# Performance work log

Measured on AMD Instinct MI355X. Metric: run time of the kernel, lower is better.

Reference implementation:

```python
import jax, jax.numpy as jnp
import numpy as np

LAMBDA_A = 1.0
NUM_ITER = 3
K = 64
BN_EPS = 1e-5


def setup_inputs() -> dict:
    key = jax.random.key(0)
    ks = jax.random.split(key, 8)
    B, C, H, W = 16, 512, 64, 64
    x = jax.random.normal(ks[0], (B, C, H, W), dtype=jnp.float32)
    # codebook mu: init normal(std~sqrt(2/k)) then L2-normalize along dim=1 (k axis), as in torch init
    mu = jax.random.normal(ks[1], (C, K), dtype=jnp.float32) * np.sqrt(2.0 / K)
    mu = mu / jnp.maximum(jnp.linalg.norm(mu, axis=1, keepdims=True), 1e-12)
    # 1x1 convs expressed as (out, in) matrices
    stem_w = jax.random.normal(ks[2], (C, C), dtype=jnp.float32) * np.sqrt(2.0 / C)
    stem_b = jnp.zeros((C,), dtype=jnp.float32)
    head_w = jax.random.normal(ks[3], (C, C), dtype=jnp.float32) * np.sqrt(2.0 / C)
    head_b = jnp.zeros((C,), dtype=jnp.float32)
    bn_gamma = jnp.ones((C,), dtype=jnp.float32)
    bn_beta = jnp.zeros((C,), dtype=jnp.float32)
    return {"x": x, "mu": mu, "stem_w": stem_w, "stem_b": stem_b,
            "head_w": head_w, "head_b": head_b,
            "bn_gamma": bn_gamma, "bn_beta": bn_beta}


def _conv1x1(x, w, b):
    # x: (B,C,H,W), w: (O,C)
    return jnp.einsum('bchw,oc->bohw', x, w) + b[None, :, None, None]


def reference(x, mu, stem_w, stem_b, head_w, head_b, bn_gamma, bn_beta):
    B, C, H, W = x.shape
    N = H * W
    y = _conv1x1(x, stem_w, stem_b)                 # (B,C,H,W)
    yf = y.reshape(B, C, N).transpose(0, 2, 1)      # (B,N,C)

    mu_b = jnp.broadcast_to(mu[None], (B, C, K))    # (B,C,K)
    z = None
    for _ in range(NUM_ITER):
        z = jax.nn.softmax(LAMBDA_A * jnp.einsum('bnc,bck->bnk', yf, mu_b), axis=2)
        zn = z / (1e-6 + z.sum(axis=1, keepdims=True))
        mu_b = jnp.einsum('bnc,bnk->bck', yf, zn)
        mu_b = mu_b / jnp.maximum(jnp.linalg.norm(mu_b, axis=1, keepdims=True), 1e-12)

    # EM loop runs under no_grad in torch
    mu_b = jax.lax.stop_gradient(mu_b)
    z = jax.lax.stop_gradient(z)

    y2 = jnp.einsum('bck,bnk->bcn', mu_b, z).reshape(B, C, H, W)

    # head: ReLU -> 1x1 conv -> BatchNorm2d (training-mode batch stats)
    h = _conv1x1(jnp.maximum(y2, 0.0), head_w, head_b)
    mean = h.mean(axis=(0, 2, 3), keepdims=True)
    var = h.var(axis=(0, 2, 3), keepdims=True)
    h = (h - mean) * jax.lax.rsqrt(var + BN_EPS)
    h = h * bn_gamma[None, :, None, None] + bn_beta[None, :, None, None]

    return jnp.maximum(h + x, 0.0)
```

## Files before the change

### kernel.cpp

```cpp
#include <hip/hip_runtime.h>


typedef _Float16 half_t;
typedef _Float16 half4 __attribute__((ext_vector_type(4)));
typedef _Float16 half8 __attribute__((ext_vector_type(8)));
typedef float f32x4 __attribute__((ext_vector_type(4)));

#define GLD_LDS(gp, lp) __builtin_amdgcn_global_load_lds( \
    (const __attribute__((address_space(1))) void*)(gp),  \
    (__attribute__((address_space(3))) void*)(lp), 16, 0, 0)

#define SBAR __builtin_amdgcn_sched_barrier(0)
#define RAWBAR do { SBAR; __builtin_amdgcn_s_barrier(); SBAR; } while (0)
#define VM0   do { asm volatile("s_waitcnt vmcnt(0)" ::: "memory"); SBAR; } while (0)

constexpr int CB = 16;
constexpr int CC = 512;
constexpr int CN = 4096;
constexpr int CKK = 64;
constexpr long MALL = (long)CB * CN;

__device__ inline int swz8(int bid, int n) {
  return (bid & 7) * (n >> 3) + (bid >> 3);
}

__global__ __launch_bounds__(256) void prep(
    const float* __restrict__ stem_w, const float* __restrict__ head_w,
    const float* __restrict__ mu,
    half_t* __restrict__ swh, half_t* __restrict__ hwh,
    half_t* __restrict__ muT, half_t* __restrict__ muck)
{
  int i = blockIdx.x * 256 + threadIdx.x;
  swh[i] = (half_t)stem_w[i];
  hwh[i] = (half_t)head_w[i];
  if (i < CC * CKK) {
    int c = i >> 6, k = i & 63;
    half_t v = (half_t)mu[i];
    for (int b = 0; b < CB; ++b) {
      muT[(long)b * CKK * CC + (long)k * CC + c] = v;
      muck[(long)b * CC * CKK + i] = v;
    }
  }
}

__global__ __launch_bounds__(256) void xpose(
    const float* __restrict__ in, half_t* __restrict__ outT)
{
  __shared__ half_t t[64][65];
  const int s0 = blockIdx.x * 64, r0 = blockIdx.y * 64;
  const long bz = blockIdx.z;
  const float* ib = in + bz * (long)CC * CN;
  half_t* ob = outT + bz * (long)CC * CN;
  const int tid = threadIdx.x, cl = tid & 63, rw = tid >> 6;
#pragma unroll
  for (int it = 0; it < 16; ++it) {
    int r = it * 4 + rw;
    t[cl][r] = (half_t)ib[(long)(r0 + r) * CN + s0 + cl];
  }
  __syncthreads();
#pragma unroll
  for (int it = 0; it < 16; ++it) {
    int s = it * 4 + rw;
    ob[(long)(s0 + s) * CC + r0 + cl] = t[s][cl];
  }
}

template <int BM, int BN, int MODE, int EPI, bool SWZ, bool STATS>
__global__ __launch_bounds__(256) void gemm_abt(
    const half_t* __restrict__ A, const half_t* __restrict__ Bm,
    half_t* __restrict__ Co, half_t* __restrict__ CoT,
    float* __restrict__ Cacc, const float* __restrict__ bias,
    float* __restrict__ stats,
    int M, int Nn, int Kk, int ksplit, long sA, long sB, long sC)
{
  constexpr int FM = BM / 32, FN = BN / 32;
  constexpr int HB = (BM + BN) * 64;
  constexpr int EPS = (EPI != 0) ? BN * (BM + 4) : 0;
  constexpr int TOT = HB > EPS ? HB : EPS;
  __shared__ __align__(16) half_t smem[TOT];

  const int tid = threadIdx.x, wid = tid >> 6, lane = tid & 63;
  int bid = blockIdx.x;
  if constexpr (SWZ) bid = swz8(bid, gridDim.x);
  const int tilesN = Nn / BN;
  const int tm = bid / tilesN, tn = bid % tilesN;
  const long bz = blockIdx.z;
  const half_t* Ab = A + bz * sA + (long)tm * BM * Kk;
  const half_t* Bb = Bm + bz * sB + (long)tn * BN * Kk;
  const int ksteps = Kk >> 6;
  const int per = ksteps / ksplit;
  const int ks0 = blockIdx.y * per, ks1 = ks0 + per;
  const int wr = wid >> 1, wc = wid & 1;

  const int r8 = lane >> 3;
  const int gcs = ((lane & 7) ^ r8) * 8;

  auto stage = [&](int ks) {
    half_t* dA = smem;
    half_t* dB = smem + BM * 64;
    const half_t* ga = Ab + (long)ks * 64;
#pragma unroll
    for (int c = wid; c < BM / 8; c += 4)
      GLD_LDS(ga + (long)(c * 8 + r8) * Kk + gcs, &dA[c * 512]);
    const half_t* gb = Bb + (long)ks * 64;
#pragma unroll
    for (int c = wid; c < BN / 8; c += 4)
      GLD_LDS(gb + (long)(c * 8 + r8) * Kk + gcs, &dB[c * 512]);
  };

  f32x4 acc[FM][FN];
#pragma unroll
  for (int i = 0; i < FM; ++i)
#pragma unroll
    for (int j = 0; j < FN; ++j) acc[i][j] = f32x4{0.f, 0.f, 0.f, 0.f};

  for (int ks = ks0; ks < ks1; ++ks) {
    stage(ks);
    VM0;
    RAWBAR;
    const half_t* lA = smem;
    const half_t* lB = smem + BM * 64;
#pragma unroll
    for (int kk = 0; kk < 2; ++kk) {
      half8 af[FM], bfr[FN];
      const int cg = kk * 4 + (lane >> 4);
#pragma unroll
      for (int i = 0; i < FM; ++i) {
        const int rA = wr * (BM / 2) + i * 16 + (lane & 15);
        af[i] = *(const half8*)&lA[rA * 64 + ((cg ^ (rA & 7)) << 3)];
      }
#pragma unroll
      for (int j = 0; j < FN; ++j) {
        const int rB = wc * (BN / 2) + j * 16 + (lane & 15);
        bfr[j] = *(const half8*)&lB[rB * 64 + ((cg ^ (rB & 7)) << 3)];
      }
      __builtin_amdgcn_s_setprio(1);
#pragma unroll
      for (int i = 0; i < FM; ++i)
#pragma unroll
        for (int j = 0; j < FN; ++j)
          acc[i][j] = __builtin_amdgcn_mfma_f32_16x16x32_f16(af[i], bfr[j],
                                                             acc[i][j], 0, 0, 0);
      __builtin_amdgcn_s_setprio(0);
    }
    RAWBAR;
  }

  if constexpr (EPI != 0) {
    static_assert(BM == 128 && BN == 128, "LDS epilogue assumes 128x128");
    constexpr int PIT = BM + 4;
    half_t* ep = smem;
#pragma unroll
    for (int j = 0; j < FN; ++j) {
      const int nl = wc * 64 + j * 16 + (lane & 15);
      float bv = 0.f;
      if constexpr (MODE & 1) bv = bias[tn * BN + nl];
      float s1 = 0.f, s2 = 0.f;
#pragma unroll
      for (int i = 0; i < FM; ++i) {
        const int ml = wr * 64 + i * 16 + ((lane >> 4) << 2);
        half4 h;
#pragma unroll
        for (int r = 0; r < 4; ++r) {
          float v = acc[i][j][r] + bv;
          if constexpr (MODE & 2) v = fmaxf(v, 0.f);
          if constexpr (STATS) { s1 += v; s2 += v * v; }
          h[r] = (half_t)v;
        }
        *(half4*)&ep[nl * PIT + ml] = h;
      }
      if constexpr (STATS) {
        s1 += __shfl_xor(s1, 16); s1 += __shfl_xor(s1, 32);
        s2 += __shfl_xor(s2, 16); s2 += __shfl_xor(s2, 32);
        if (lane < 16) {
          const int ch = tn * BN + nl;
          atomicAdd(&stats[ch], s1);
          atomicAdd(&stats[CC + ch], s2);
        }
      }
    }
    __syncthreads();
    const long rowbase = (long)tm * BM;
    if constexpr (EPI & 1) {
#pragma unroll
      for (int s = 0; s < 8; ++s) {
        const int q = tid + 256 * s;
        const int m = q & 127, cc8 = q >> 7;
        half8 v;
#pragma unroll
        for (int e = 0; e < 8; ++e) v[e] = ep[(cc8 * 8 + e) * PIT + m];
        *(half8*)&Co[bz * sC + (rowbase + m) * Nn + tn * BN + cc8 * 8] = v;
      }
    }
    if constexpr (EPI & 2) {
      const long b = rowbase >> 12, nbase = rowbase & 4095;
#pragma unroll
      for (int s = 0; s < 8; ++s) {
        const int q = tid + 256 * s;
        const int mc = q & 15, cl = q >> 4;
        half8 v = *(const half8*)&ep[cl * PIT + mc * 8];
        *(half8*)&CoT[(b * Nn + tn * BN + cl) * 4096 + nbase + mc * 8] = v;
      }
    }
  } else {
#pragma unroll
    for (int j = 0; j < FN; ++j) {
      const int n = tn * BN + wc * (BN / 2) + j * 16 + (lane & 15);
      float bv = 0.f;
      if constexpr (MODE & 1) bv = bias[n];
#pragma unroll
      for (int i = 0; i < FM; ++i) {
        const int mbase = tm * BM + wr * (BM / 2) + i * 16 + ((lane >> 4) << 2);
#pragma unroll
        for (int r = 0; r < 4; ++r) {
          const long idx = bz * sC + (long)(mbase + r) * Nn + n;
          if constexpr ((MODE & 4) != 0) {
            atomicAdd(&Cacc[idx], acc[i][j][r]);
          } else {
            float v = acc[i][j][r] + bv;
            if constexpr ((MODE & 2) != 0) v = fmaxf(v, 0.f);
            Co[idx] = (half_t)v;
          }
        }
      }
    }
  }
}

__global__ __launch_bounds__(256) void s_softmax(
    const half_t* __restrict__ Yf, const half_t* __restrict__ muT,
    half_t* __restrict__ zp, half_t* __restrict__ zT)
{
  constexpr int HB = (128 + 64) * 64;
  __shared__ __align__(16) union {
    half_t st[HB];
    half_t zh[128 * 68];
  } sm;
  const int tid = threadIdx.x, wid = tid >> 6, lane = tid & 63;
  const int tm = blockIdx.x;
  const long bz = blockIdx.z;
  const half_t* Ab = Yf + bz * (long)CN * CC + (long)tm * 128 * CC;
  const half_t* Bb = muT + bz * (long)CKK * CC;

  const int r8 = lane >> 3;
  const int gcs = ((lane & 7) ^ r8) * 8;

  auto stage = [&](int ks) {
    half_t* dA = sm.st;
    half_t* dB = sm.st + 128 * 64;
    const half_t* ga = Ab + (long)ks * 64;
#pragma unroll
    for (int c = wid; c < 16; c += 4)
      GLD_LDS(ga + (long)(c * 8 + r8) * CC + gcs, &dA[c * 512]);
    const half_t* gb = Bb + (long)ks * 64;
#pragma unroll
    for (int c = wid; c < 8; c += 4)
      GLD_LDS(gb + (long)(c * 8 + r8) * CC + gcs, &dB[c * 512]);
  };

  f32x4 acc[2][4];
#pragma unroll
  for (int i = 0; i < 2; ++i)
#pragma unroll
    for (int j = 0; j < 4; ++j) acc[i][j] = f32x4{0.f, 0.f, 0.f, 0.f};

  for (int ks = 0; ks < 8; ++ks) {
    stage(ks);
    VM0;
    RAWBAR;
    const half_t* lA = sm.st;
    const half_t* lB = sm.st + 128 * 64;
#pragma unroll
    for (int kk = 0; kk < 2; ++kk) {
      half8 af[2], bfr[4];
      const int cg = kk * 4 + (lane >> 4);
#pragma unroll
      for (int i = 0; i < 2; ++i) {
        const int rA = wid * 32 + i * 16 + (lane & 15);
        af[i] = *(const half8*)&lA[rA * 64 + ((cg ^ (rA & 7)) << 3)];
      }
#pragma unroll
      for (int j = 0; j < 4; ++j) {
        const int rB = j * 16 + (lane & 15);
        bfr[j] = *(const half8*)&lB[rB * 64 + ((cg ^ (rB & 7)) << 3)];
      }
      __builtin_amdgcn_s_setprio(1);
#pragma unroll
      for (int i = 0; i < 2; ++i)
#pragma unroll
        for (int j = 0; j < 4; ++j)
          acc[i][j] = __builtin_amdgcn_mfma_f32_16x16x32_f16(af[i], bfr[j],
                                                             acc[i][j], 0, 0, 0);
      __builtin_amdgcn_s_setprio(0);
    }
    RAWBAR;
  }

#pragma unroll
  for (int i = 0; i < 2; ++i)
#pragma unroll
    for (int r = 0; r < 4; ++r) {
      float mx = fmaxf(fmaxf(acc[i][0][r], acc[i][1][r]),
                       fmaxf(acc[i][2][r], acc[i][3][r]));
#pragma unroll
      for (int m = 1; m < 16; m <<= 1) mx = fmaxf(mx, __shfl_xor(mx, m));
      float p[4], s = 0.f;
#pragma unroll
      for (int j = 0; j < 4; ++j) { p[j] = __expf(acc[i][j][r] - mx); s += p[j]; }
#pragma unroll
      for (int m = 1; m < 16; m <<= 1) s += __shfl_xor(s, m);
      const float inv = 1.f / s;
#pragma unroll
      for (int j = 0; j < 4; ++j) acc[i][j][r] = p[j] * inv;
    }

#pragma unroll
  for (int i = 0; i < 2; ++i)
#pragma unroll
    for (int j = 0; j < 4; ++j)
#pragma unroll
      for (int r = 0; r < 4; ++r) {
        const int row = wid * 32 + i * 16 + ((lane >> 4) << 2) + r;
        const int col = j * 16 + (lane & 15);
        sm.zh[row * 68 + col] = (half_t)acc[i][j][r];
      }
  __syncthreads();
  if (zp) {
    const int nl = tid >> 1, seg = tid & 1;
    const long base = bz * (long)CN * CKK + (long)(tm * 128 + nl) * CKK + seg * 32;
#pragma unroll
    for (int g = 0; g < 4; ++g) {
      half8 v;
#pragma unroll
      for (int e = 0; e < 8; ++e) v[e] = sm.zh[nl * 68 + seg * 32 + g * 8 + e];
      *(half8*)&zp[base + g * 8] = v;
    }
  }
  {
    const int k = tid >> 2, seg = tid & 3;
    const long base = bz * (long)CKK * CN + (long)k * CN + tm * 128 + seg * 32;
#pragma unroll
    for (int g = 0; g < 4; ++g) {
      half8 v;
#pragma unroll
      for (int e = 0; e < 8; ++e) v[e] = sm.zh[(seg * 32 + g * 8 + e) * 68 + k];
      *(half8*)&zT[base + g * 8] = v;
    }
  }
}

__global__ __launch_bounds__(64) void mu_norm(
    const float* __restrict__ acc, half_t* __restrict__ muT, half_t* __restrict__ muck)
{
  const int bk = blockIdx.x;
  const int b = bk >> 6, k = bk & 63;
  const float* row = acc + (long)bk * CC;
  const int t = threadIdx.x;
  float v[8]; float s = 0.f;
#pragma unroll
  for (int e = 0; e < 8; ++e) { v[e] = row[t * 8 + e]; s += v[e] * v[e]; }
#pragma unroll
  for (int m = 1; m < 64; m <<= 1) s += __shfl_xor(s, m);
  const float inv = 1.f / fmaxf(sqrtf(s), 1e-12f);
  half8 o;
#pragma unroll
  for (int e = 0; e < 8; ++e) o[e] = (half_t)(v[e] * inv);
  *(half8*)&muT[(long)bk * CC + t * 8] = o;
  half_t* mc = muck + (long)b * CC * CKK;
#pragma unroll
  for (int e = 0; e < 8; ++e) mc[(long)(t * 8 + e) * CKK + k] = o[e];
}

__global__ void bn_param(const float* __restrict__ stats,
                         const float* __restrict__ gamma, const float* __restrict__ beta,
                         float* __restrict__ scsh)
{
  const int c = threadIdx.x;
  const float cnt = 1.f / 65536.f;
  const float mean = stats[c] * cnt;
  const float var = stats[CC + c] * cnt - mean * mean;
  const float sc = gamma[c] * rsqrtf(var + 1e-5f);
  scsh[c] = sc;
  scsh[CC + c] = beta[c] - mean * sc;
}

__global__ __launch_bounds__(256) void bn_final2(
    const half_t* __restrict__ hcn, const float* __restrict__ x,
    const float* __restrict__ scsh, float* __restrict__ out)
{
  const long i8 = (long)blockIdx.x * 256 + threadIdx.x;
  const int c = (int)((i8 >> 9) & 511);
  const float sc = scsh[c], sh = scsh[CC + c];
  half8 h = *(const half8*)&hcn[i8 * 8];
  f32x4 x0 = *(const f32x4*)&x[i8 * 8];
  f32x4 x1 = *(const f32x4*)&x[i8 * 8 + 4];
  f32x4 o0, o1;
#pragma unroll
  for (int e = 0; e < 4; ++e) o0[e] = fmaxf((float)h[e] * sc + sh + x0[e], 0.f);
#pragma unroll
  for (int e = 0; e < 4; ++e) o1[e] = fmaxf((float)h[4 + e] * sc + sh + x1[e], 0.f);
  *(f32x4*)&out[i8 * 8] = o0;
  *(f32x4*)&out[i8 * 8 + 4] = o1;
}

extern "C" void kernel_launch(void* const* d_in, const int* in_sizes, int n_in,
                              void* d_out, int out_size, void* d_ws, size_t ws_size,
                              hipStream_t stream)
{
  const float* x      = (const float*)d_in[0];
  const float* mu     = (const float*)d_in[1];
  const float* stem_w = (const float*)d_in[2];
  const float* stem_b = (const float*)d_in[3];
  const float* head_w = (const float*)d_in[4];
  const float* head_b = (const float*)d_in[5];
  const float* bn_g   = (const float*)d_in[6];
  const float* bn_b   = (const float*)d_in[7];
  float* out = (float*)d_out;

  const size_t NEED = 214ull << 20;
  if (ws_size < NEED) {
    hipMemsetAsync(d_out, 0, (size_t)out_size * 4, stream);
    return;
  }
  char* ws = (char*)d_ws;
  const long MB = 1 << 20;
  half_t* xT   = (half_t*)(ws);
  half_t* Yf   = (half_t*)(ws + 64 * MB);
  half_t* ycn  = (half_t*)(ws + 128 * MB);
  half_t* z    = (half_t*)(ws + 192 * MB);
  half_t* zT   = (half_t*)(ws + 200 * MB);
  half_t* muT  = (half_t*)(ws + 208 * MB);
  half_t* muck = (half_t*)(ws + 209 * MB);
  float* muacc = (float*)(ws + 210 * MB);
  half_t* swh  = (half_t*)(ws + 212 * MB);
  half_t* hwh  = (half_t*)(ws + 212 * MB + 512 * 1024);
  float* stats = (float*)(ws + 213 * MB);
  float* scsh  = (float*)(ws + 213 * MB + 8 * 1024);
  half_t* y2f = xT;
  half_t* hcn = Yf;

  prep<<<1024, 256, 0, stream>>>(stem_w, head_w, mu, swh, hwh, muT, muck);
  xpose<<<dim3(64, 8, 16), 256, 0, stream>>>(x, xT);
  gemm_abt<128, 128, 1, 3, true, false><<<dim3(2048, 1, 1), 256, 0, stream>>>(
      xT, swh, Yf, ycn, nullptr, stem_b, nullptr, (int)MALL, CC, CC, 1, 0, 0, 0);

  for (int it = 0; it < 3; ++it) {
    s_softmax<<<dim3(32, 1, 16), 256, 0, stream>>>(
        Yf, muT, (it == 2) ? z : nullptr, zT);
    hipMemsetAsync(muacc, 0, (size_t)CB * CKK * CC * 4, stream);
    gemm_abt<64, 128, 4, 0, false, false><<<dim3(4, 8, 16), 256, 0, stream>>>(
        zT, ycn, nullptr, nullptr, muacc, nullptr, nullptr, CKK, CC, CN, 8,
        (long)CKK * CN, (long)CC * CN, (long)CKK * CC);
    mu_norm<<<CB * CKK, 64, 0, stream>>>(muacc, muT, muck);
  }
  gemm_abt<128, 128, 2, 1, true, false><<<dim3(128, 1, 16), 256, 0, stream>>>(
      z, muck, y2f, nullptr, nullptr, nullptr, nullptr, CN, CC, CKK, 1,
      (long)CN * CKK, (long)CC * CKK, (long)CN * CC);
  hipMemsetAsync(stats, 0, 2 * CC * sizeof(float), stream);
  gemm_abt<128, 128, 1, 2, true, true><<<dim3(2048, 1, 1), 256, 0, stream>>>(
      y2f, hwh, nullptr, hcn, nullptr, head_b, stats, (int)MALL, CC, CC, 1, 0, 0, 0);

  bn_param<<<1, 512, 0, stream>>>(stats, bn_g, bn_b, scsh);
  bn_final2<<<16384, 256, 0, stream>>>(hcn, x, scsh, out);
}
```

Before: 421.1 us.

## Add 256x256-tile 512-thread GEMM for stem and head 1x1 convolutions

Adds a dedicated gemm512 kernel with 256x256 output tiles, 8 waves, swizzled double-buffered LDS staging via global_load_lds and a two-pass LDS epilogue. It replaces the 128x128 gemm_abt for the stem and head convolutions, raising operand reuse and cutting redundant global loads. The head pass now computes BN statistics from fp32 accumulators before the fp16 rounding. Separately, the mu-update GEMM's split-K drops from 8 to 4, halving atomic adds at the cost of fewer blocks. The 64KB+ LDS footprint and large accumulator array may limit occupancy.

```diff
diff --git a/kernel.cpp b/kernel.cpp
--- a/kernel.cpp
+++ b/kernel.cpp
@@ -65,12 +65,160 @@
   }
 }
 
-template <int BM, int BN, int MODE, int EPI, bool SWZ, bool STATS>
+template <bool WN, bool STATS>
+__global__ __launch_bounds__(512, 2) void gemm512(
+    const half_t* __restrict__ A, const half_t* __restrict__ Bw,
+    const float* __restrict__ bias,
+    half_t* __restrict__ Co, half_t* __restrict__ CoT,
+    float* __restrict__ stats)
+{
+  __shared__ __align__(16) half_t smem[65536];
+  const int tid = threadIdx.x, wid = tid >> 6, lane = tid & 63;
+  const int bid = swz8(blockIdx.x, gridDim.x);
+  const int tm = bid >> 1, tn = bid & 1;
+  const long row0 = (long)tm * 256;
+  const int wr = wid >> 2, wc = wid & 3;
+  const int r8 = lane >> 3;
+  const int gcs = ((lane & 7) ^ r8) * 8;
+
+  const half_t* Ab = A + row0 * 512;
+  const half_t* Bb = Bw + (long)tn * 256 * 512;
+
+  auto stageA = [&](int t, int buf) {
+    half_t* dA = smem + buf * 32768;
+    const half_t* g = Ab + t * 64;
+#pragma unroll
+    for (int c = wid; c < 32; c += 8)
+      GLD_LDS(g + (long)(c * 8 + r8) * 512 + gcs, &dA[c * 512]);
+  };
+  auto stageB = [&](int t, int buf) {
+    half_t* dB = smem + buf * 32768 + 16384;
+    const half_t* g = Bb + t * 64;
+#pragma unroll
+    for (int c = wid; c < 32; c += 8)
+      GLD_LDS(g + (long)(c * 8 + r8) * 512 + gcs, &dB[c * 512]);
+  };
+
+  f32x4 acc[8][4];
+#pragma unroll
+  for (int i = 0; i < 8; ++i)
+#pragma unroll
+    for (int j = 0; j < 4; ++j) acc[i][j] = f32x4{0.f, 0.f, 0.f, 0.f};
+
+  stageA(0, 0);
+  stageB(0, 0);
+  VM0;
+  RAWBAR;
+
+  for (int t = 0; t < 8; ++t) {
+    const int cur = t & 1;
+    const half_t* lA = smem + cur * 32768;
+    const half_t* lB = lA + 16384;
+#pragma unroll
+    for (int ph = 0; ph < 4; ++ph) {
+      const int mh = ph >> 1, kh = ph & 1;
+      const int cg = kh * 4 + (lane >> 4);
+      half8 af[4], bf[4];
+#pragma unroll
+      for (int i = 0; i < 4; ++i) {
+        const int rA = wr * 128 + mh * 64 + i * 16 + (lane & 15);
+        af[i] = *(const half8*)&lA[rA * 64 + ((cg ^ (rA & 7)) << 3)];
+      }
+#pragma unroll
+      for (int j = 0; j < 4; ++j) {
+        const int rB = wc * 64 + j * 16 + (lane & 15);
+        bf[j] = *(const half8*)&lB[rB * 64 + ((cg ^ (rB & 7)) << 3)];
+      }
+      if (ph == 0 && t < 7) stageA(t + 1, cur ^ 1);
+      if (ph == 1 && t < 7) stageB(t + 1, cur ^ 1);
+      RAWBAR;
+      __builtin_amdgcn_s_setprio(1);
+#pragma unroll
+      for (int i = 0; i < 4; ++i)
+#pragma unroll
+        for (int j = 0; j < 4; ++j)
+          acc[mh * 4 + i][j] = __builtin_amdgcn_mfma_f32_16x16x32_f16(
+              af[i], bf[j], acc[mh * 4 + i][j], 0, 0, 0);
+      __builtin_amdgcn_s_setprio(0);
+      if (ph == 3 && t < 7) { asm volatile("s_waitcnt vmcnt(0)" ::: "memory"); SBAR; }
+      RAWBAR;
+    }
+  }
+
+  if constexpr (STATS) {
+#pragma unroll
+    for (int j = 0; j < 4; ++j) {
+      const float bv = bias[tn * 256 + wc * 64 + j * 16 + (lane & 15)];
+      float s1 = 0.f, s2 = 0.f;
+#pragma unroll
+      for (int i8 = 0; i8 < 8; ++i8)
+#pragma unroll
+        for (int r = 0; r < 4; ++r) {
+          float v = acc[i8][j][r] + bv;
+          s1 += v; s2 += v * v;
+        }
+      s1 += __shfl_xor(s1, 16); s1 += __shfl_xor(s1, 32);
+      s2 += __shfl_xor(s2, 16); s2 += __shfl_xor(s2, 32);
+      if (lane < 16) {
+        const int ch = tn * 256 + wc * 64 + j * 16 + lane;
+        atomicAdd(&stats[ch], s1);
+        atomicAdd(&stats[CC + ch], s2);
+      }
+    }
+  }
+
+  constexpr int PIT = 260;
+  half_t* ep = smem;
+  const long b = row0 >> 12;
+  const int nbase = (int)(row0 & 4095);
+#pragma unroll
+  for (int nh = 0; nh < 2; ++nh) {
+    __syncthreads();
+    if ((wc >> 1) == nh) {
+#pragma unroll
+      for (int j = 0; j < 4; ++j) {
+        const int nl = (wc & 1) * 64 + j * 16 + (lane & 15);
+        const float bv = bias[tn * 256 + nh * 128 + nl];
+#pragma unroll
+        for (int i8 = 0; i8 < 8; ++i8) {
+          const int ml = wr * 128 + i8 * 16 + ((lane >> 4) << 2);
+          half4 h;
+#pragma unroll
+          for (int r = 0; r < 4; ++r) h[r] = (half_t)(acc[i8][j][r] + bv);
+          *(half4*)&ep[nl * PIT + ml] = h;
+        }
+      }
+    }
+    __syncthreads();
+    if constexpr (WN) {
+#pragma unroll
+      for (int s = 0; s < 8; ++s) {
+        const int q = tid + 512 * s;
+        const int m = q & 255, ch = q >> 8;
+        half8 v;
+#pragma unroll
+        for (int e = 0; e < 8; ++e) v[e] = ep[(ch * 8 + e) * PIT + m];
+        *(half8*)&Co[(row0 + m) * 512 + tn * 256 + nh * 128 + ch * 8] = v;
+      }
+    }
+    {
+#pragma unroll
+      for (int s = 0; s < 8; ++s) {
+        const int q = tid + 512 * s;
+        const int cl = q >> 5, mc = q & 31;
+        half8 v = *(const half8*)&ep[cl * PIT + mc * 8];
+        *(half8*)&CoT[(b * 512 + tn * 256 + nh * 128 + cl) * 4096 +
+                      nbase + mc * 8] = v;
+      }
+    }
+  }
+}
+
+template <int BM, int BN, int MODE, int EPI, bool SWZ>
 __global__ __launch_bounds__(256) void gemm_abt(
     const half_t* __restrict__ A, const half_t* __restrict__ Bm,
-    half_t* __restrict__ Co, half_t* __restrict__ CoT,
-    float* __restrict__ Cacc, const float* __restrict__ bias,
-    float* __restrict__ stats,
+    half_t* __restrict__ Co, float* __restrict__ Cacc,
+    const float* __restrict__ bias,
     int M, int Nn, int Kk, int ksplit, long sA, long sB, long sC)
 {
   constexpr int FM = BM / 32, FN = BN / 32;
@@ -155,7 +303,6 @@
       const int nl = wc * 64 + j * 16 + (lane & 15);
       float bv = 0.f;
       if constexpr (MODE & 1) bv = bias[tn * BN + nl];
-      float s1 = 0.f, s2 = 0.f;
 #pragma unroll
       for (int i = 0; i < FM; ++i) {
         const int ml = wr * 64 + i * 16 + ((lane >> 4) << 2);
@@ -164,43 +311,21 @@
         for (int r = 0; r < 4; ++r) {
           float v = acc[i][j][r] + bv;
           if constexpr (MODE & 2) v = fmaxf(v, 0.f);
-          if constexpr (STATS) { s1 += v; s2 += v * v; }
           h[r] = (half_t)v;
         }
         *(half4*)&ep[nl * PIT + ml] = h;
       }
-      if constexpr (STATS) {
-        s1 += __shfl_xor(s1, 16); s1 += __shfl_xor(s1, 32);
-        s2 += __shfl_xor(s2, 16); s2 += __shfl_xor(s2, 32);
-        if (lane < 16) {
-          const int ch = tn * BN + nl;
-          atomicAdd(&stats[ch], s1);
-          atomicAdd(&stats[CC + ch], s2);
-        }
-      }
     }
     __syncthreads();
     const long rowbase = (long)tm * BM;
-    if constexpr (EPI & 1) {
-#pragma unroll
-      for (int s = 0; s < 8; ++s) {
-        const int q = tid + 256 * s;
-        const int m = q & 127, cc8 = q >> 7;
-        half8 v;
-#pragma unroll
-        for (int e = 0; e < 8; ++e) v[e] = ep[(cc8 * 8 + e) * PIT + m];
-        *(half8*)&Co[bz * sC + (rowbase + m) * Nn + tn * BN + cc8 * 8] = v;
-      }
-    }
-    if constexpr (EPI & 2) {
-      const long b = rowbase >> 12, nbase = rowbase & 4095;
-#pragma unroll
-      for (int s = 0; s < 8; ++s) {
-        const int q = tid + 256 * s;
-        const int mc = q & 15, cl = q >> 4;
-        half8 v = *(const half8*)&ep[cl * PIT + mc * 8];
-        *(half8*)&CoT[(b * Nn + tn * BN + cl) * 4096 + nbase + mc * 8] = v;
-      }
+#pragma unroll
+    for (int s = 0; s < 8; ++s) {
+      const int q = tid + 256 * s;
+      const int m = q & 127, cc8 = q >> 7;
+      half8 v;
+#pragma unroll
+      for (int e = 0; e < 8; ++e) v[e] = ep[(cc8 * 8 + e) * PIT + m];
+      *(half8*)&Co[bz * sC + (rowbase + m) * Nn + tn * BN + cc8 * 8] = v;
     }
   } else {
 #pragma unroll
@@ -441,24 +566,24 @@
 
   prep<<<1024, 256, 0, stream>>>(stem_w, head_w, mu, swh, hwh, muT, muck);
   xpose<<<dim3(64, 8, 16), 256, 0, stream>>>(x, xT);
-  gemm_abt<128, 128, 1, 3, true, false><<<dim3(2048, 1, 1), 256, 0, stream>>>(
-      xT, swh, Yf, ycn, nullptr, stem_b, nullptr, (int)MALL, CC, CC, 1, 0, 0, 0);
+  gemm512<true, false><<<512, 512, 0, stream>>>(
+      xT, swh, stem_b, Yf, ycn, nullptr);
 
   for (int it = 0; it < 3; ++it) {
     s_softmax<<<dim3(32, 1, 16), 256, 0, stream>>>(
         Yf, muT, (it == 2) ? z : nullptr, zT);
     hipMemsetAsync(muacc, 0, (size_t)CB * CKK * CC * 4, stream);
-    gemm_abt<64, 128, 4, 0, false, false><<<dim3(4, 8, 16), 256, 0, stream>>>(
-        zT, ycn, nullptr, nullptr, muacc, nullptr, nullptr, CKK, CC, CN, 8,
+    gemm_abt<64, 128, 4, 0, false><<<dim3(4, 4, 16), 256, 0, stream>>>(
+        zT, ycn, nullptr, muacc, nullptr, CKK, CC, CN, 4,
         (long)CKK * CN, (long)CC * CN, (long)CKK * CC);
     mu_norm<<<CB * CKK, 64, 0, stream>>>(muacc, muT, muck);
   }
-  gemm_abt<128, 128, 2, 1, true, false><<<dim3(128, 1, 16), 256, 0, stream>>>(
-      z, muck, y2f, nullptr, nullptr, nullptr, nullptr, CN, CC, CKK, 1,
+  gemm_abt<128, 128, 2, 1, true><<<dim3(128, 1, 16), 256, 0, stream>>>(
+      z, muck, y2f, nullptr, nullptr, CN, CC, CKK, 1,
       (long)CN * CKK, (long)CC * CKK, (long)CN * CC);
   hipMemsetAsync(stats, 0, 2 * CC * sizeof(float), stream);
-  gemm_abt<128, 128, 1, 2, true, true><<<dim3(2048, 1, 1), 256, 0, stream>>>(
-      y2f, hwh, nullptr, hcn, nullptr, head_b, stats, (int)MALL, CC, CC, 1, 0, 0, 0);
+  gemm512<false, true><<<512, 512, 0, stream>>>(
+      y2f, hwh, head_b, nullptr, hcn, stats);
 
   bn_param<<<1, 512, 0, stream>>>(stats, bn_g, bn_b, scsh);
   bn_final2<<<16384, 256, 0, stream>>>(hcn, x, scsh, out);
```

Measured after the change: 416.6 us. About the same (-1.1%).
